# Kernel tuning notes

Hardware: AMD Instinct MI355X
Metric: run time of the kernel (lower is better)

Reference implementation:

```python
import jax, jax.numpy as jnp
import numpy as np
from jax import lax

B, C_IN, H, W = 128, 3, 32, 32
HC, HHC, P, NCLS = 32, 128, 4, 10
STEPS_PER_PIECE = 1           # fixed-step RK4: 1 step per unit-length piece
DT = 1.0 / STEPS_PER_PIECE
DIMNUMS = ('NCHW', 'OIHW', 'NCHW')


def setup_inputs() -> dict:
    key = jax.random.key(0)
    ks = jax.random.split(key, 8)
    def rn(k, shape, fan_in):
        return jax.random.normal(k, shape, jnp.float32) / np.sqrt(fan_in).astype(np.float32)
    return {
        'x': jax.random.normal(ks[0], (B, C_IN, H, W), jnp.float32),
        'y': jax.random.randint(ks[1], (B,), 0, NCLS),
        'aug_W': rn(ks[2], (HC, C_IN), C_IN),
        'aug_b': jnp.zeros((HC,), jnp.float32),
        'W1': rn(ks[3], (P, HHC, 1 + HC), 1 + HC),      # stacked 1x1 conv weights per piece
        'b1': jnp.zeros((P, HHC), jnp.float32),
        'W2': rn(ks[4], (P, HHC, HHC, 3, 3), HHC * 9),  # stacked 3x3 conv weights per piece
        'b2': jnp.zeros((P, HHC), jnp.float32),
        'W3': rn(ks[5], (P, HC, HHC), HHC),             # stacked 1x1 conv weights per piece
        'b3': jnp.zeros((P, HC), jnp.float32),
        'ro_W': rn(ks[6], (NCLS, HC * H * W), HC * H * W),
        'ro_b': jnp.zeros((NCLS,), jnp.float32),
    }


def _func(t, z, W1, b1, W2, b2, W3, b3):
    # piece selection: bisect(range(P+1), t) - 1, clipped -> floor(t) clipped to [0, P-1]
    idx = jnp.clip(jnp.floor(t).astype(jnp.int32), 0, P - 1)
    w1, v1 = W1[idx], b1[idx]
    w2, v2 = W2[idx], b2[idx]
    w3, v3 = W3[idx], b3[idx]
    # broadcast time as an extra channel and concat: [B, 1+HC, H, W]
    tc = jnp.full((z.shape[0], 1, z.shape[2], z.shape[3]), t, z.dtype)
    h = jnp.concatenate([tc, z], axis=1)
    h = jax.nn.softplus(jnp.einsum('bchw,oc->bohw', h, w1) + v1[:, None, None])
    h = lax.conv_general_dilated(h, w2, (1, 1), 'SAME', dimension_numbers=DIMNUMS)
    h = jax.nn.softplus(h + v2[None, :, None, None])
    h = jnp.einsum('bchw,oc->bohw', h, w3) + v3[:, None, None]
    return jnp.tanh(h)  # tanh=True


def reference(x, y, aug_W, aug_b, W1, b1, W2, b2, W3, b3, ro_W, ro_b):
    # augment: Linear over channel dim (transpose(1,3) trick == 1x1 conv)
    z = jnp.einsum('bchw,oc->bohw', x, aug_W) + aug_b[:, None, None]

    def f(t, zz):
        return _func(t, zz, W1, b1, W2, b2, W3, b3)

    dt = jnp.float32(DT)
    t0s = jnp.arange(P * STEPS_PER_PIECE, dtype=jnp.float32) * dt

    def rk4_step(zz, t0):
        k1 = f(t0, zz)
        k2 = f(t0 + dt / 2, zz + (dt / 2) * k1)
        k3 = f(t0 + dt / 2, zz + (dt / 2) * k2)
        k4 = f(t0 + dt, zz + dt * k3)
        return zz + (dt / 6) * (k1 + 2 * k2 + 2 * k3 + k4), None

    zT, _ = lax.scan(rk4_step, z, t0s)

    logits = zT.reshape(zT.shape[0], -1) @ ro_W.T + ro_b
    logp = jax.nn.log_softmax(logits, axis=-1)
    loss = -jnp.mean(jnp.take_along_axis(logp, y[:, None], axis=1))
    accuracy = (jnp.argmax(logits, axis=1) == y).sum().astype(logits.dtype)
    return loss, accuracy
```

## Files before the change

kernel.cpp:

```cpp
#include <hip/hip_runtime.h>
#include <hip/hip_bf16.h>
#include <math.h>

#define BN   128
#define CIN  3
#define HCn  32
#define HHCn 128
#define NPX  1024
#define PN   4
#define NCLS 10

#define PPAD  204
#define PPADR 208
#define NT    13
#define PLROW 8
#define PLSZ  1664
#define H2P   136

typedef short bf16x8 __attribute__((ext_vector_type(8)));
typedef float f32x4  __attribute__((ext_vector_type(4)));

__device__ __forceinline__ float softplus_f(float x) {
    return fmaxf(x, 0.f) + __logf(1.f + __expf(-fabsf(x)));
}
__device__ __forceinline__ float tanh_fast(float x) {
    float e = __expf(-2.f * fabsf(x));
    float r = 1.f - 2.f * e * __builtin_amdgcn_rcpf(1.f + e);
    unsigned u = (__float_as_uint(r) & 0x7fffffffu) | (__float_as_uint(x) & 0x80000000u);
    return __uint_as_float(u);
}
__device__ __forceinline__ unsigned int f2bf(float f) {
    unsigned int u = __float_as_uint(f);
    return (u + 0x7fffu + ((u >> 16) & 1u)) >> 16;
}
__device__ __forceinline__ float bf2f(unsigned int h) {
    return __uint_as_float(h << 16);
}
__device__ __forceinline__ void pack2(float a, float b, unsigned int& hi, unsigned int& lo) {
    __hip_bfloat162 h2 = __float22bfloat162_rn(float2{a, b});
    unsigned int h = *reinterpret_cast<unsigned int*>(&h2);
    float ha = __uint_as_float(h << 16);
    float hb = __uint_as_float(h & 0xffff0000u);
    __hip_bfloat162 l2 = __float22bfloat162_rn(float2{a - ha, b - hb});
    hi = h;
    lo = *reinterpret_cast<unsigned int*>(&l2);
}

__global__ __launch_bounds__(256) void k_aug(
    const float* __restrict__ x, const float* __restrict__ aW,
    const float* __restrict__ ab, float* __restrict__ z)
{
    const int b = blockIdx.x, tid = threadIdx.x;
    const size_t xb = (size_t)b * CIN * NPX;
    const size_t zb = (size_t)b * HCn * NPX;
    float xv[CIN][4];
#pragma unroll
    for (int c = 0; c < CIN; c++)
#pragma unroll
        for (int j = 0; j < 4; j++)
            xv[c][j] = x[xb + c * NPX + tid + 256 * j];
    for (int o = 0; o < HCn; o++) {
        float w0 = aW[o * 3], w1 = aW[o * 3 + 1], w2 = aW[o * 3 + 2], bb = ab[o];
#pragma unroll
        for (int j = 0; j < 4; j++) {
            float v = fmaf(w0, xv[0][j], fmaf(w1, xv[1][j], fmaf(w2, xv[2][j], bb)));
            z[zb + (size_t)o * NPX + tid + 256 * j] = v;
        }
    }
}

__global__ __launch_bounds__(256) void k_packW2(
    const float* __restrict__ W2, unsigned short* __restrict__ whi,
    unsigned short* __restrict__ wlo)
{
    int t = blockIdx.x * 256 + threadIdx.x;
    int j    = t & 7;
    int lane = (t >> 3) & 63;
    int ocg  = (t >> 9) & 7;
    int kc   = (t >> 12) & 3;
    int p9s  = t >> 14;
    int sh = p9s % 9, p = p9s / 9;
    int dy = sh / 3, dx = sh % 3;
    int oc = ocg * 16 + (lane & 15);
    int ic = kc * 32 + (lane >> 4) * 8 + j;
    float v = W2[((((size_t)p * HHCn + oc) * HHCn + ic) * 3 + dy) * 3 + dx];
    unsigned int hi = f2bf(v);
    whi[t] = (unsigned short)hi;
    wlo[t] = (unsigned short)f2bf(v - bf2f(hi));
}

__global__ __launch_bounds__(256) void k_packW1(
    const float* __restrict__ W1, unsigned short* __restrict__ whi,
    unsigned short* __restrict__ wlo)
{
    int t = blockIdx.x * 256 + threadIdx.x;
    int j = t & 7, lane = (t >> 3) & 63, m = (t >> 9) & 1, kc = (t >> 10) & 3, p = t >> 12;
    int oc = kc * 32 + m * 16 + (lane & 15);
    int ic = (lane >> 4) * 8 + j;
    float v = W1[((size_t)p * HHCn + oc) * 33 + 1 + ic];
    unsigned int hi = f2bf(v);
    whi[t] = (unsigned short)hi;
    wlo[t] = (unsigned short)f2bf(v - bf2f(hi));
}

__global__ __launch_bounds__(256) void k_packW3(
    const float* __restrict__ W3, unsigned short* __restrict__ whi,
    unsigned short* __restrict__ wlo)
{
    int t = blockIdx.x * 256 + threadIdx.x;
    int j = t & 7, lane = (t >> 3) & 63, kk = (t >> 9) & 3, m = (t >> 11) & 1, p = t >> 12;
    int st = m * 16 + (lane & 15);
    int ic = kk * 32 + (lane >> 4) * 8 + j;
    float v = W3[((size_t)p * HCn + st) * HHCn + ic];
    unsigned int hi = f2bf(v);
    whi[t] = (unsigned short)hi;
    wlo[t] = (unsigned short)f2bf(v - bf2f(hi));
}

__global__ __launch_bounds__(512, 4) void k_fused(
    const float* __restrict__ z_in, const float* __restrict__ kb_in, float alpha,
    const float* __restrict__ b1p, const float* __restrict__ W1t, float t,
    const unsigned short* __restrict__ w1h, const unsigned short* __restrict__ w1l,
    const unsigned short* __restrict__ w2h, const unsigned short* __restrict__ w2l,
    const float* __restrict__ b2p,
    const unsigned short* __restrict__ w3h, const unsigned short* __restrict__ w3l,
    const float* __restrict__ b3p,
    float* __restrict__ kb_out, float* __restrict__ accb, float* __restrict__ z_out,
    int mode)
{
    const int strip = blockIdx.x, b = blockIdx.y;
    const int tid = threadIdx.x, lane = tid & 63, wid = tid >> 6;
    const int ln15 = lane & 15, lg = lane >> 4;
    const int kl8 = lg * 8, kl4 = lg * 4;

    __shared__ __align__(16) unsigned short S[26624];
    unsigned short* zinh = S;
    unsigned short* zinl = S + 6656;
    unsigned short* xh   = S + 13312;
    unsigned short* xl   = S + 19968;
    unsigned short* h2qh = S;
    unsigned short* h2ql = S + 8704;

    const size_t zbB = (size_t)b * HCn * NPX;
    const int strip0 = strip * 4;

    {
        const int ic0 = wid * 4;
        const int pl  = wid >> 1;
        const int sl  = (wid & 1) * 4;
#pragma unroll
        for (int it = 0; it < 4; it++) {
            int ppad = it * 64 + lane;
            int prow = ppad / 34, pcol = ppad - prow * 34;
            int gy = strip0 + prow - 1, gx = pcol - 1;
            bool okm = (ppad < PPAD) && (gy >= 0) && (gy < 32) && (gx >= 0) && (gx < 32);
            int gsrc = gy * 32 + gx;
            float v[4];
#pragma unroll
            for (int c = 0; c < 4; c++)
                v[c] = okm ? z_in[zbB + (size_t)(ic0 + c) * NPX + gsrc] : 0.f;
            if (alpha != 0.f) {
#pragma unroll
                for (int c = 0; c < 4; c++)
                    if (okm) v[c] = fmaf(alpha, kb_in[zbB + (size_t)(ic0 + c) * NPX + gsrc], v[c]);
            }
            unsigned int h01, l01, h23, l23;
            pack2(v[0], v[1], h01, l01);
            pack2(v[2], v[3], h23, l23);
            if (ppad < PPADR) {
                int off = pl * PLSZ + ppad * PLROW + sl;
                *(uint2*)(zinh + off) = make_uint2(h01, h23);
                *(uint2*)(zinl + off) = make_uint2(l01, l23);
            }
        }
    }
    __syncthreads();

    const int wocg = (wid & 3) * 2;
    const int wph  = (wid >> 2) * 64;
    int boff[4];
#pragma unroll
    for (int f = 0; f < 4; f++) {
        int pxl = wph + f * 16 + ln15;
        boff[f] = lg * PLSZ + ((pxl >> 5) * 34 + (pxl & 31)) * PLROW;
    }

    f32x4 acc[2][4];
#pragma unroll
    for (int o = 0; o < 2; o++)
#pragma unroll
        for (int f = 0; f < 4; f++) acc[o][f] = (f32x4)(0.f);

    for (int kc = 0; kc < 4; kc++) {
        const unsigned short* w1hb = w1h + (size_t)kc * 1024 + lane * 8;
        const unsigned short* w1lb = w1l + (size_t)kc * 1024 + lane * 8;
        bf16x8 a1h0 = *(const bf16x8*)w1hb,          a1h1 = *(const bf16x8*)(w1hb + 512);
        bf16x8 a1l0 = *(const bf16x8*)w1lb,          a1l1 = *(const bf16x8*)(w1lb + 512);
        f32x4 c1[2][2];
#pragma unroll
        for (int m = 0; m < 2; m++)
#pragma unroll
            for (int ni = 0; ni < 2; ni++) c1[m][ni] = (f32x4)(0.f);
#pragma unroll
        for (int ni = 0; ni < 2; ni++) {
            int n = wid + 8 * ni;
            if (ni == 0 || wid < 5) {
                int roff = lg * PLSZ + (n * 16 + ln15) * PLROW;
                bf16x8 bh = *(const bf16x8*)(zinh + roff);
                bf16x8 bl = *(const bf16x8*)(zinl + roff);
                c1[0][ni] = __builtin_amdgcn_mfma_f32_16x16x32_bf16(a1h0, bh, c1[0][ni], 0, 0, 0);
                c1[0][ni] = __builtin_amdgcn_mfma_f32_16x16x32_bf16(a1h0, bl, c1[0][ni], 0, 0, 0);
                c1[0][ni] = __builtin_amdgcn_mfma_f32_16x16x32_bf16(a1l0, bh, c1[0][ni], 0, 0, 0);
                c1[1][ni] = __builtin_amdgcn_mfma_f32_16x16x32_bf16(a1h1, bh, c1[1][ni], 0, 0, 0);
                c1[1][ni] = __builtin_amdgcn_mfma_f32_16x16x32_bf16(a1h1, bl, c1[1][ni], 0, 0, 0);
                c1[1][ni] = __builtin_amdgcn_mfma_f32_16x16x32_bf16(a1l1, bh, c1[1][ni], 0, 0, 0);
            }
        }
        float eb[2][4];
#pragma unroll
        for (int m = 0; m < 2; m++)
#pragma unroll
            for (int r = 0; r < 4; r++) {
                int oc = kc * 32 + m * 16 + kl4 + r;
                eb[m][r] = b1p[oc] + t * W1t[oc * 33];
            }
        __syncthreads();
#pragma unroll
        for (int ni = 0; ni < 2; ni++) {
            int n = wid + 8 * ni;
            if (ni == 0 || wid < 5) {
                int ppad = n * 16 + ln15;
                int prow = ppad / 34, pcol = ppad - prow * 34;
                int gy = strip0 + prow - 1;
                bool zero = (pcol == 0) || (pcol == 33) || (gy < 0) || (gy >= 32);
#pragma unroll
                for (int m = 0; m < 2; m++) {
                    float v[4];
#pragma unroll
                    for (int r = 0; r < 4; r++)
                        v[r] = zero ? 0.f : softplus_f(c1[m][ni][r] + eb[m][r]);
                    unsigned int h01, l01, h23, l23;
                    pack2(v[0], v[1], h01, l01);
                    pack2(v[2], v[3], h23, l23);
                    int off = (m * 2 + (kl4 >> 3)) * PLSZ + ppad * PLROW + (kl4 & 7);
                    *(uint2*)(xh + off) = make_uint2(h01, h23);
                    *(uint2*)(xl + off) = make_uint2(l01, l23);
                }
            }
        }
        __syncthreads();
#pragma unroll
        for (int sh = 0; sh < 9; sh++) {
            const size_t wbase = ((size_t)(sh * 4 + kc) * 8 + wocg) * 512 + lane * 8;
            bf16x8 ah0 = *(const bf16x8*)(w2h + wbase);
            bf16x8 al0 = *(const bf16x8*)(w2l + wbase);
            bf16x8 ah1 = *(const bf16x8*)(w2h + wbase + 512);
            bf16x8 al1 = *(const bf16x8*)(w2l + wbase + 512);
            const int soff = ((sh / 3) * 34 + (sh % 3)) * PLROW;
#pragma unroll
            for (int f = 0; f < 4; f++) {
                bf16x8 bh = *(const bf16x8*)(xh + boff[f] + soff);
                bf16x8 bl = *(const bf16x8*)(xl + boff[f] + soff);
                acc[0][f] = __builtin_amdgcn_mfma_f32_16x16x32_bf16(ah0, bh, acc[0][f], 0, 0, 0);
                acc[0][f] = __builtin_amdgcn_mfma_f32_16x16x32_bf16(ah0, bl, acc[0][f], 0, 0, 0);
                acc[0][f] = __builtin_amdgcn_mfma_f32_16x16x32_bf16(al0, bh, acc[0][f], 0, 0, 0);
                acc[1][f] = __builtin_amdgcn_mfma_f32_16x16x32_bf16(ah1, bh, acc[1][f], 0, 0, 0);
                acc[1][f] = __builtin_amdgcn_mfma_f32_16x16x32_bf16(ah1, bl, acc[1][f], 0, 0, 0);
                acc[1][f] = __builtin_amdgcn_mfma_f32_16x16x32_bf16(al1, bh, acc[1][f], 0, 0, 0);
            }
        }
    }

    float bb2[2][4];
#pragma unroll
    for (int o2 = 0; o2 < 2; o2++)
#pragma unroll
        for (int r = 0; r < 4; r++)
            bb2[o2][r] = b2p[(wocg + o2) * 16 + kl4 + r];

    const size_t obB = (size_t)b * HCn * NPX + strip * 128;
    const int m3 = wid & 1, n4 = wid >> 1;
    float bb3[4];
#pragma unroll
    for (int r = 0; r < 4; r++) bb3[r] = b3p[m3 * 16 + kl4 + r];

#pragma unroll
    for (int q = 0; q < 2; q++) {
        __syncthreads();
        if ((wid >> 2) == q) {
#pragma unroll
            for (int o2 = 0; o2 < 2; o2++)
#pragma unroll
                for (int f2 = 0; f2 < 4; f2++) {
                    f32x4 a = acc[o2][f2];
                    float v[4];
#pragma unroll
                    for (int r = 0; r < 4; r++) v[r] = softplus_f(a[r] + bb2[o2][r]);
                    unsigned int h01, l01, h23, l23;
                    pack2(v[0], v[1], h01, l01);
                    pack2(v[2], v[3], h23, l23);
                    int off = (f2 * 16 + ln15) * H2P + (wocg + o2) * 16 + kl4;
                    *(uint2*)(h2qh + off) = make_uint2(h01, h23);
                    *(uint2*)(h2ql + off) = make_uint2(l01, l23);
                }
        }
        __syncthreads();
        f32x4 c3 = (f32x4)(0.f);
#pragma unroll
        for (int kk = 0; kk < 4; kk++) {
            const unsigned short* a3hb = w3h + (size_t)(m3 * 4 + kk) * 512 + lane * 8;
            const unsigned short* a3lb = w3l + (size_t)(m3 * 4 + kk) * 512 + lane * 8;
            bf16x8 a3h = *(const bf16x8*)a3hb;
            bf16x8 a3l = *(const bf16x8*)a3lb;
            bf16x8 bh = *(const bf16x8*)(h2qh + (n4 * 16 + ln15) * H2P + kk * 32 + kl8);
            bf16x8 bl = *(const bf16x8*)(h2ql + (n4 * 16 + ln15) * H2P + kk * 32 + kl8);
            c3 = __builtin_amdgcn_mfma_f32_16x16x32_bf16(a3h, bh, c3, 0, 0, 0);
            c3 = __builtin_amdgcn_mfma_f32_16x16x32_bf16(a3h, bl, c3, 0, 0, 0);
            c3 = __builtin_amdgcn_mfma_f32_16x16x32_bf16(a3l, bh, c3, 0, 0, 0);
        }
#pragma unroll
        for (int r = 0; r < 4; r++) {
            int st = m3 * 16 + kl4 + r;
            float v = tanh_fast(c3[r] + bb3[r]);
            size_t i = obB + (size_t)st * NPX + q * 64 + n4 * 16 + ln15;
            if (mode == 0)      { kb_out[i] = v; accb[i] = v; }
            else if (mode == 1) { kb_out[i] = v; accb[i] += 2.f * v; }
            else                { z_out[i] = z_in[i] + (accb[i] + v) * (1.f / 6.f); }
        }
    }
}

__global__ __launch_bounds__(256) void k_logits(
    const float* __restrict__ z, const float* __restrict__ roW,
    const float* __restrict__ rob, float* __restrict__ logits)
{
    const int b = blockIdx.x, tid = threadIdx.x;
    float p[NCLS];
#pragma unroll
    for (int c = 0; c < NCLS; c++) p[c] = 0.f;
    const float* zp = z + (size_t)b * 32768;
    for (int i = tid; i < 32768; i += 256) {
        float zv = zp[i];
#pragma unroll
        for (int c = 0; c < NCLS; c++) p[c] = fmaf(zv, roW[(size_t)c * 32768 + i], p[c]);
    }
#pragma unroll
    for (int c = 0; c < NCLS; c++)
        for (int off = 32; off > 0; off >>= 1) p[c] += __shfl_down(p[c], off, 64);
    __shared__ float red[4][NCLS];
    int wid = tid >> 6, lane = tid & 63;
    if (lane == 0)
#pragma unroll
        for (int c = 0; c < NCLS; c++) red[wid][c] = p[c];
    __syncthreads();
    if (tid < NCLS) {
        float s = red[0][tid] + red[1][tid] + red[2][tid] + red[3][tid] + rob[tid];
        logits[b * NCLS + tid] = s;
    }
}

__global__ __launch_bounds__(128) void k_loss(
    const float* __restrict__ logits, const int* __restrict__ y,
    float* __restrict__ out)
{
    const int b = threadIdx.x;
    float l[NCLS];
#pragma unroll
    for (int c = 0; c < NCLS; c++) l[c] = logits[b * NCLS + c];
    float m = l[0]; int am = 0;
#pragma unroll
    for (int c = 1; c < NCLS; c++) if (l[c] > m) { m = l[c]; am = c; }
    float s = 0.f;
#pragma unroll
    for (int c = 0; c < NCLS; c++) s += expf(l[c] - m);
    float lse = m + logf(s);
    int yy = y[b];
    float loss_b = lse - l[yy];
    float corr = (am == yy) ? 1.f : 0.f;
    for (int off = 32; off > 0; off >>= 1) {
        loss_b += __shfl_down(loss_b, off, 64);
        corr   += __shfl_down(corr,   off, 64);
    }
    __shared__ float sl[2], sc[2];
    if ((b & 63) == 0) { sl[b >> 6] = loss_b; sc[b >> 6] = corr; }
    __syncthreads();
    if (b == 0) {
        out[0] = (sl[0] + sl[1]) / (float)BN;
        out[1] = sc[0] + sc[1];
    }
}

extern "C" void kernel_launch(void* const* d_in, const int* in_sizes, int n_in,
                              void* d_out, int out_size, void* d_ws, size_t ws_size,
                              hipStream_t stream) {
    const float* x   = (const float*)d_in[0];
    const int*   y   = (const int*)  d_in[1];
    const float* aW  = (const float*)d_in[2];
    const float* ab  = (const float*)d_in[3];
    const float* W1  = (const float*)d_in[4];
    const float* b1  = (const float*)d_in[5];
    const float* W2  = (const float*)d_in[6];
    const float* b2  = (const float*)d_in[7];
    const float* W3  = (const float*)d_in[8];
    const float* b3  = (const float*)d_in[9];
    const float* roW = (const float*)d_in[10];
    const float* rob = (const float*)d_in[11];
    float* out = (float*)d_out;
    float* ws  = (float*)d_ws;

    const size_t ZSZ = (size_t)BN * HCn * NPX;
    float* zb0    = ws;
    float* zb1    = zb0 + ZSZ;
    float* kb0    = zb1 + ZSZ;
    float* kb1    = kb0 + ZSZ;
    float* accb   = kb1 + ZSZ;
    float* logits = accb + ZSZ;
    unsigned short* w2h = (unsigned short*)(logits + 4096);
    unsigned short* w2l = w2h + 589824;
    unsigned short* w1h = w2l + 589824;
    unsigned short* w1l = w1h + 16384;
    unsigned short* w3h = w1l + 16384;
    unsigned short* w3l = w3h + 16384;

    k_packW2<<<2304, 256, 0, stream>>>(W2, w2h, w2l);
    k_packW1<<<64, 256, 0, stream>>>(W1, w1h, w1l);
    k_packW3<<<64, 256, 0, stream>>>(W3, w3h, w3l);
    k_aug<<<BN, 256, 0, stream>>>(x, aW, ab, zb0);

    float* zA = zb0;
    float* zB = zb1;
    for (int p = 0; p < PN; p++) {
        for (int e = 0; e < 4; e++) {
            const int idx = (e == 3 && p + 1 < PN) ? p + 1 : p;
            const float t = (float)p + (e == 0 ? 0.f : (e == 3 ? 1.f : 0.5f));
            const float alpha = (e == 0) ? 0.f : (e == 3 ? 1.f : 0.5f);
            const int mode = (e == 0) ? 0 : (e == 3 ? 2 : 1);
            const float* kbin = (e == 2) ? kb1 : kb0;
            float* kbout = (e == 1) ? kb1 : kb0;
            k_fused<<<dim3(8, BN), 512, 0, stream>>>(
                zA, kbin, alpha,
                b1 + (size_t)idx * HHCn, W1 + (size_t)idx * HHCn * 33, t,
                w1h + (size_t)idx * 4096, w1l + (size_t)idx * 4096,
                w2h + (size_t)idx * 147456, w2l + (size_t)idx * 147456,
                b2 + (size_t)idx * HHCn,
                w3h + (size_t)idx * 4096, w3l + (size_t)idx * 4096,
                b3 + (size_t)idx * HCn,
                kbout, accb, zB, mode);
        }
        float* tmp = zA; zA = zB; zB = tmp;
    }

    k_logits<<<BN, 256, 0, stream>>>(zA, roW, rob, logits);
    k_loss<<<1, 128, 0, stream>>>(logits, y, out);
}
```

Baseline: 1.998 ms.

## Double-buffer conv1 output in LDS to overlap with 3x3 conv MFMAs

Splits the per-channel-chunk loop into conv1, softplus-write and 3x3-conv stages, and adds a second LDS buffer for the intermediate activations. The next chunk's conv1 and write now run alongside the current chunk's 3x3 conv, which cuts the barriers per chunk from two to one. The goal is to hide barrier stalls and let MFMA work from different stages interleave. In exchange, shared memory per block grows by about half, which lowers the number of resident blocks per CU.

```diff
diff --git a/kernel.cpp b/kernel.cpp
--- a/kernel.cpp
+++ b/kernel.cpp
@@ -12,7 +12,6 @@
 
 #define PPAD  204
 #define PPADR 208
-#define NT    13
 #define PLROW 8
 #define PLSZ  1664
 #define H2P   136
@@ -133,11 +132,13 @@
     const int ln15 = lane & 15, lg = lane >> 4;
     const int kl8 = lg * 8, kl4 = lg * 4;
 
-    __shared__ __align__(16) unsigned short S[26624];
+    __shared__ __align__(16) unsigned short S[39936];
     unsigned short* zinh = S;
     unsigned short* zinl = S + 6656;
-    unsigned short* xh   = S + 13312;
-    unsigned short* xl   = S + 19968;
+    unsigned short* xh0  = S + 13312;
+    unsigned short* xl0  = S + 19968;
+    unsigned short* xh1  = S + 26624;
+    unsigned short* xl1  = S + 33280;
     unsigned short* h2qh = S;
     unsigned short* h2ql = S + 8704;
 
@@ -174,7 +175,6 @@
             }
         }
     }
-    __syncthreads();
 
     const int wocg = (wid & 3) * 2;
     const int wph  = (wid >> 2) * 64;
@@ -191,12 +191,13 @@
 #pragma unroll
         for (int f = 0; f < 4; f++) acc[o][f] = (f32x4)(0.f);
 
-    for (int kc = 0; kc < 4; kc++) {
+    f32x4 c1[2][2];
+
+    auto do_conv1 = [&](int kc) {
         const unsigned short* w1hb = w1h + (size_t)kc * 1024 + lane * 8;
         const unsigned short* w1lb = w1l + (size_t)kc * 1024 + lane * 8;
-        bf16x8 a1h0 = *(const bf16x8*)w1hb,          a1h1 = *(const bf16x8*)(w1hb + 512);
-        bf16x8 a1l0 = *(const bf16x8*)w1lb,          a1l1 = *(const bf16x8*)(w1lb + 512);
-        f32x4 c1[2][2];
+        bf16x8 a1h0 = *(const bf16x8*)w1hb, a1h1 = *(const bf16x8*)(w1hb + 512);
+        bf16x8 a1l0 = *(const bf16x8*)w1lb, a1l1 = *(const bf16x8*)(w1lb + 512);
 #pragma unroll
         for (int m = 0; m < 2; m++)
 #pragma unroll
@@ -216,6 +217,9 @@
                 c1[1][ni] = __builtin_amdgcn_mfma_f32_16x16x32_bf16(a1l1, bh, c1[1][ni], 0, 0, 0);
             }
         }
+    };
+
+    auto do_writeX = [&](int kc, unsigned short* xh_, unsigned short* xl_) {
         float eb[2][4];
 #pragma unroll
         for (int m = 0; m < 2; m++)
@@ -224,7 +228,6 @@
                 int oc = kc * 32 + m * 16 + kl4 + r;
                 eb[m][r] = b1p[oc] + t * W1t[oc * 33];
             }
-        __syncthreads();
 #pragma unroll
         for (int ni = 0; ni < 2; ni++) {
             int n = wid + 8 * ni;
@@ -243,12 +246,14 @@
                     pack2(v[0], v[1], h01, l01);
                     pack2(v[2], v[3], h23, l23);
                     int off = (m * 2 + (kl4 >> 3)) * PLSZ + ppad * PLROW + (kl4 & 7);
-                    *(uint2*)(xh + off) = make_uint2(h01, h23);
-                    *(uint2*)(xl + off) = make_uint2(l01, l23);
+                    *(uint2*)(xh_ + off) = make_uint2(h01, h23);
+                    *(uint2*)(xl_ + off) = make_uint2(l01, l23);
                 }
             }
         }
-        __syncthreads();
+    };
+
+    auto do_conv3 = [&](int kc, const unsigned short* xh_, const unsigned short* xl_) {
 #pragma unroll
         for (int sh = 0; sh < 9; sh++) {
             const size_t wbase = ((size_t)(sh * 4 + kc) * 8 + wocg) * 512 + lane * 8;
@@ -259,8 +264,8 @@
             const int soff = ((sh / 3) * 34 + (sh % 3)) * PLROW;
 #pragma unroll
             for (int f = 0; f < 4; f++) {
-                bf16x8 bh = *(const bf16x8*)(xh + boff[f] + soff);
-                bf16x8 bl = *(const bf16x8*)(xl + boff[f] + soff);
+                bf16x8 bh = *(const bf16x8*)(xh_ + boff[f] + soff);
+                bf16x8 bl = *(const bf16x8*)(xl_ + boff[f] + soff);
                 acc[0][f] = __builtin_amdgcn_mfma_f32_16x16x32_bf16(ah0, bh, acc[0][f], 0, 0, 0);
                 acc[0][f] = __builtin_amdgcn_mfma_f32_16x16x32_bf16(ah0, bl, acc[0][f], 0, 0, 0);
                 acc[0][f] = __builtin_amdgcn_mfma_f32_16x16x32_bf16(al0, bh, acc[0][f], 0, 0, 0);
@@ -269,7 +274,20 @@
                 acc[1][f] = __builtin_amdgcn_mfma_f32_16x16x32_bf16(al1, bh, acc[1][f], 0, 0, 0);
             }
         }
-    }
+    };
+
+    __syncthreads();
+    do_conv1(0);
+    do_writeX(0, xh0, xl0);
+    __syncthreads();
+
+    do_conv1(1); do_writeX(1, xh1, xl1); do_conv3(0, xh0, xl0);
+    __syncthreads();
+    do_conv1(2); do_writeX(2, xh0, xl0); do_conv3(1, xh1, xl1);
+    __syncthreads();
+    do_conv1(3); do_writeX(3, xh1, xl1); do_conv3(2, xh0, xl0);
+    __syncthreads();
+    do_conv3(3, xh1, xl1);
 
     float bb2[2][4];
 #pragma unroll
```

Result: no change. 1.992 ms (-0.3%).
